# Kernel optimization log

Measured on AMD Instinct MI355X. Metric: run time of the kernel, lower is better.

The kernel has to match this reference:

```python
import jax, jax.numpy as jnp
import numpy as np

N_RAYS = 8192
M = 524288
GX, GY, GZ = 160, 160, 128
NFEAT = 12
POS_PE, VIEW_PE = 10, 4
WIDTH = 128
POS_DIM = 3 + 3 * POS_PE * 2      # 63
VIEW_DIM = 3 + 3 * VIEW_PE * 2    # 27
DIM0 = NFEAT + POS_DIM            # 75
ACT_SHIFT = float(np.log(1.0 / (1.0 - 1e-6) - 1.0))  # density bias shift from alpha_init
INTERVAL = 0.5                    # stepsize * voxel_size_ratio
XYZ_MIN, XYZ_MAX = -1.0, 1.0


def posemb(x, n_pe):
    # x: [N,3] -> [N, 3 + 3*n_pe*2], matching cat([x, sin(x*freq), cos(x*freq)])
    freq = 2.0 ** jnp.arange(n_pe, dtype=x.dtype)
    xf = (x[..., None] * freq).reshape(x.shape[0], -1)
    return jnp.concatenate([x, jnp.sin(xf), jnp.cos(xf)], axis=-1)


def trilinear(grid, xyz):
    # grid: [X,Y,Z,C]; xyz: [M,3] in world coords. align_corners=True bilinear (grid_sample).
    sz_f = jnp.array(grid.shape[:3], jnp.float32)
    sz_i = jnp.array(grid.shape[:3], jnp.int32)
    t = (xyz - XYZ_MIN) / (XYZ_MAX - XYZ_MIN) * (sz_f - 1.0)
    t = jnp.clip(t, 0.0, sz_f - 1.0)
    i0 = jnp.clip(jnp.floor(t).astype(jnp.int32), 0, sz_i - 2)
    f = t - i0.astype(t.dtype)
    out = jnp.zeros((xyz.shape[0], grid.shape[-1]), t.dtype)
    for dx in (0, 1):
        for dy in (0, 1):
            for dz in (0, 1):
                w = ((f[:, 0] if dx else 1.0 - f[:, 0])
                     * (f[:, 1] if dy else 1.0 - f[:, 1])
                     * (f[:, 2] if dz else 1.0 - f[:, 2]))
                out = out + w[:, None] * grid[i0[:, 0] + dx, i0[:, 1] + dy, i0[:, 2] + dz]
    return out


def mask_lookup(mask, xyz):
    # nearest-neighbor maskcache_lookup: ijk = round(xyz*scale + shift)
    sz_f = jnp.array(mask.shape, jnp.float32)
    scale = (sz_f - 1.0) / (XYZ_MAX - XYZ_MIN)
    shift = -XYZ_MIN * scale
    ijk = jnp.clip(jnp.round(xyz * scale + shift).astype(jnp.int32), 0,
                   jnp.array(mask.shape, jnp.int32) - 1)
    return mask[ijk[:, 0], ijk[:, 1], ijk[:, 2]]


def alphas2weights(alpha, ray_id, n_rays):
    # segmented T_i = prod_{j<i in ray}(1-alpha_j); weights = T*alpha (ray_id sorted)
    log1a = jnp.log(jnp.clip(1.0 - alpha, 1e-10, 1.0))
    excl = jnp.cumsum(log1a) - log1a                      # global exclusive cumsum
    seg_tot = jax.ops.segment_sum(log1a, ray_id, num_segments=n_rays)
    seg_start = jnp.cumsum(seg_tot) - seg_tot             # exclusive prefix over rays
    T = jnp.exp(excl - seg_start[ray_id])
    weights = T * alpha
    alphainv_last = jnp.exp(seg_tot)
    return weights, alphainv_last


def setup_inputs() -> dict:
    key = jax.random.key(0)
    ks = jax.random.split(key, 16)
    xyz = jax.random.uniform(ks[0], (M, 3), jnp.float32) * (XYZ_MAX - XYZ_MIN) + XYZ_MIN
    ray_id = jnp.sort(jax.random.randint(ks[1], (M,), 0, N_RAYS))
    viewdirs = jax.random.normal(ks[2], (N_RAYS, 3), jnp.float32)
    viewdirs = viewdirs / jnp.linalg.norm(viewdirs, axis=-1, keepdims=True)
    mask = jax.random.uniform(ks[3], (GX, GY, GZ)) > 0.1
    density = jax.random.normal(ks[4], (GX, GY, GZ), jnp.float32) * 0.5
    k0 = jax.random.normal(ks[5], (GX, GY, GZ, NFEAT), jnp.float32) * 0.1
    s = 0.05
    W0 = jax.random.normal(ks[6], (DIM0, WIDTH), jnp.float32) * s
    b0 = jnp.zeros((WIDTH,), jnp.float32)
    W1 = jax.random.normal(ks[7], (WIDTH, WIDTH), jnp.float32) * s
    b1 = jnp.zeros((WIDTH,), jnp.float32)
    W2 = jax.random.normal(ks[8], (WIDTH, WIDTH), jnp.float32) * s
    b2 = jnp.zeros((WIDTH,), jnp.float32)
    Wr = jax.random.normal(ks[9], (WIDTH + VIEW_DIM, 3), jnp.float32) * s
    br = jnp.zeros((3,), jnp.float32)
    return {"xyz": xyz, "ray_id": ray_id, "viewdirs": viewdirs, "mask": mask,
            "density": density, "k0": k0, "W0": W0, "b0": b0, "W1": W1, "b1": b1,
            "W2": W2, "b2": b2, "Wr": Wr, "br": br}


def reference(xyz, ray_id, viewdirs, mask, density, k0, W0, b0, W1, b1, W2, b2, Wr, br):
    # 1) empty-space skipping via mask cache (kept as multiplicative mask for static shapes)
    m = mask_lookup(mask, xyz).astype(xyz.dtype)
    # 2) trilinear density query + raw2alpha
    d = trilinear(density[..., None], xyz)[:, 0]
    alpha = 1.0 - (1.0 + jnp.exp(d + ACT_SHIFT)) ** (-INTERVAL)
    alpha = alpha * m
    # 3) segmented alpha compositing (Alphas2Weights)
    weights, alphainv_last = alphas2weights(alpha, ray_id, N_RAYS)
    # 4) feature query + view MLP -> rgb
    feat = trilinear(k0, xyz)                              # [M, NFEAT]
    h = jnp.concatenate([feat, posemb(xyz, POS_PE)], -1)   # [M, DIM0]
    h = jax.nn.relu(h @ W0 + b0)
    h = jax.nn.relu(h @ W1 + b1)
    h = jax.nn.relu(h @ W2 + b2)
    ve = posemb(viewdirs, VIEW_PE)[ray_id]                 # [M, VIEW_DIM]
    rgb = jax.nn.sigmoid(jnp.concatenate([h, ve], -1) @ Wr + br)
    # 5) composite per ray + white background
    rgb_marched = jax.ops.segment_sum(weights[:, None] * rgb, ray_id, num_segments=N_RAYS)
    rgb_marched = rgb_marched + alphainv_last[:, None] * 1.0
    return rgb_marched
```

## Files before the change

### kernel.cpp

```cpp
#include <hip/hip_runtime.h>
#include <hip/hip_bf16.h>

#define M_SAMPLES 524288
#define NRAYS 8192
#define GXD 160
#define GYD 160
#define GZD 128
#define GYZ (GYD*GZD)
#define NVOX (GXD*GYD*GZD)
#define ACT_SHIFT -13.81550955796f
#define ROWA 136
#define ROWB 168

typedef __bf16 bf16x8 __attribute__((ext_vector_type(8)));
typedef float f32x4 __attribute__((ext_vector_type(4)));
typedef float f32x16 __attribute__((ext_vector_type(16)));
typedef float f32v2 __attribute__((ext_vector_type(2)));

static __device__ inline unsigned short f2bf(float f){
  __hip_bfloat16 h = __float2bfloat16(f);
  unsigned short u; __builtin_memcpy(&u, &h, 2); return u;
}
static __device__ inline float flo(unsigned int u){ return __uint_as_float(u << 16); }
static __device__ inline float fhi(unsigned int u){ return __uint_as_float(u & 0xffff0000u); }

#if defined(__has_builtin)
#if __has_builtin(__builtin_amdgcn_cvt_pk_bf16_f32)
#define HAVE_PK_BF16 1
#endif
#if __has_builtin(__builtin_amdgcn_cvt_pk_f32_fp8) && __has_builtin(__builtin_amdgcn_cvt_pk_fp8_f32)
#define HAVE_FP8 1
#endif
#endif

static __device__ inline unsigned int packbf(float a, float b){
#ifdef HAVE_PK_BF16
  typedef __bf16 bf16v2 __attribute__((ext_vector_type(2)));
  bf16v2 r = __builtin_amdgcn_cvt_pk_bf16_f32(a, b);
  unsigned int u; __builtin_memcpy(&u, &r, 4); return u;
#else
  return (unsigned int)f2bf(a) | ((unsigned int)f2bf(b) << 16);
#endif
}

struct Tri {
  int ix, iy, iz;
  float wx0, wx1, wy0, wy1, wz0, wz1;
};
static __device__ inline Tri tri_setup(float x, float y, float z){
  Tri t;
  float tx = (x+1.f)*0.5f*(float)(GXD-1); tx = fminf(fmaxf(tx,0.f),(float)(GXD-1));
  float ty = (y+1.f)*0.5f*(float)(GYD-1); ty = fminf(fmaxf(ty,0.f),(float)(GYD-1));
  float tz = (z+1.f)*0.5f*(float)(GZD-1); tz = fminf(fmaxf(tz,0.f),(float)(GZD-1));
  t.ix = min((int)tx, GXD-2); t.iy = min((int)ty, GYD-2); t.iz = min((int)tz, GZD-2);
  float fx = tx-t.ix, fy = ty-t.iy, fz = tz-t.iz;
  t.wx0 = 1.f-fx; t.wx1 = fx; t.wy0 = 1.f-fy; t.wy1 = fy; t.wz0 = 1.f-fz; t.wz1 = fz;
  return t;
}

__global__ __launch_bounds__(256) void k_prep(const unsigned int* __restrict__ mw,
    int* __restrict__ flag,
    const float* __restrict__ W0, const float* __restrict__ W1,
    const float* __restrict__ W2, const float* __restrict__ Wr,
    unsigned short* __restrict__ wt0, unsigned short* __restrict__ wt1,
    unsigned short* __restrict__ wt2, unsigned short* __restrict__ wtr,
    const float* __restrict__ vd, float* __restrict__ ve)
{
  int b = blockIdx.x;
  if(b == 0){
    unsigned int v = mw[threadIdx.x & 63];
    unsigned long long any = __ballot(v > 1u);
    if(threadIdx.x == 0) *flag = (any != 0ull) ? 1 : 0;
    return;
  }
  if(b < 187){
    int t = (b-1)*256 + threadIdx.x;
    if(t < 128*96){
      int n = t/96, k = t%96;
      wt0[t] = f2bf((k < 75) ? W0[k*128 + n] : 0.f);
    } else if(t < 128*96 + 16384){
      int j = t - 128*96; int n = j/128, k = j%128;
      wt1[j] = f2bf(W1[k*128 + n]);
    } else if(t < 128*96 + 32768){
      int j = t - 128*96 - 16384; int n = j/128, k = j%128;
      wt2[j] = f2bf(W2[k*128 + n]);
    } else if(t < 128*96 + 32768 + 16*160){
      int j = t - 128*96 - 32768; int n = j/160, k = j%160;
      wtr[j] = f2bf((n < 3 && k < 155) ? Wr[k*3 + n] : 0.f);
    }
    return;
  }
  int t = (b-187)*256 + threadIdx.x;
  if(t >= NRAYS*27) return;
  int ray = t/27, c = t%27;
  float v;
  if(c < 3) v = vd[ray*3 + c];
  else if(c < 15){
    int q = c - 3; int ci = q/4, p = q%4;
    v = sinf(vd[ray*3 + ci] * (float)(1 << p));
  } else {
    int q = c - 15; int ci = q/4, p = q%4;
    v = cosf(vd[ray*3 + ci] * (float)(1 << p));
  }
  ve[t] = v;
}

#ifdef HAVE_FP8
__global__ __launch_bounds__(256) void k_repack(const float* __restrict__ density,
    const float* __restrict__ k0, uint4* __restrict__ packed)
{
  int v = blockIdx.x*256 + threadIdx.x;
  if(v >= NVOX) return;
  const float4* kp = (const float4*)(k0 + (size_t)v*12);
  float4 a = kp[0], b = kp[1], c = kp[2];
  uint4 o;
  o.x = __float_as_uint(density[v]);
  int w;
  w = __builtin_amdgcn_cvt_pk_fp8_f32(a.x, a.y, 0, false);
  w = __builtin_amdgcn_cvt_pk_fp8_f32(a.z, a.w, w, true);
  o.y = (unsigned int)w;
  w = __builtin_amdgcn_cvt_pk_fp8_f32(b.x, b.y, 0, false);
  w = __builtin_amdgcn_cvt_pk_fp8_f32(b.z, b.w, w, true);
  o.z = (unsigned int)w;
  w = __builtin_amdgcn_cvt_pk_fp8_f32(c.x, c.y, 0, false);
  w = __builtin_amdgcn_cvt_pk_fp8_f32(c.z, c.w, w, true);
  o.w = (unsigned int)w;
  packed[v] = o;
}
#else
__global__ __launch_bounds__(256) void k_repack(const float* __restrict__ density,
    const float* __restrict__ k0, uint4* __restrict__ packed)
{
  int v = blockIdx.x*256 + threadIdx.x;
  if(v >= NVOX) return;
  const float4* kp = (const float4*)(k0 + (size_t)v*12);
  float4 a = kp[0], b = kp[1], c = kp[2];
  uint4 o0, o1;
  o0.x = __float_as_uint(density[v]);
  o0.y = packbf(a.x, a.y); o0.z = packbf(a.z, a.w); o0.w = packbf(b.x, b.y);
  o1.x = packbf(b.z, b.w); o1.y = packbf(c.x, c.y); o1.z = packbf(c.z, c.w);
  o1.w = 0;
  packed[(size_t)v*2]   = o0;
  packed[(size_t)v*2+1] = o1;
}
#endif

template<int KDIM, int SROW, int DROW>
static __device__ inline void layer32(const unsigned short* src, unsigned short* dst,
    const unsigned short* __restrict__ wt, const float* __restrict__ bias,
    int wave, int ln, int kh)
{
  constexpr int NS = KDIM/16;
  int tile_s = wave & 1, tile_n = wave >> 1;
  const unsigned short* wbase = wt + (tile_n*32 + ln)*KDIM + kh*8;
  const unsigned short* abase = src + (tile_s*32 + ln)*SROW + kh*8;
  f32x16 acc = {0.f,0.f,0.f,0.f,0.f,0.f,0.f,0.f,0.f,0.f,0.f,0.f,0.f,0.f,0.f,0.f};
  #pragma unroll
  for(int st = 0; st < NS; ++st){
    bf16x8 af = *(const bf16x8*)(wbase + st*16);
    bf16x8 bfr = *(const bf16x8*)(abase + st*16);
    acc = __builtin_amdgcn_mfma_f32_32x32x16_bf16(af, bfr, acc, 0, 0, 0);
  }
  int scol = tile_s*32 + ln;
  #pragma unroll
  for(int g = 0; g < 4; ++g){
    int n0 = tile_n*32 + g*8 + kh*4;
    float4 bv = *(const float4*)(bias + n0);
    unsigned int lo = packbf(fmaxf(acc[4*g+0] + bv.x, 0.f), fmaxf(acc[4*g+1] + bv.y, 0.f));
    unsigned int hi = packbf(fmaxf(acc[4*g+2] + bv.z, 0.f), fmaxf(acc[4*g+3] + bv.w, 0.f));
    unsigned long long o = (unsigned long long)lo | ((unsigned long long)hi << 32);
    *(unsigned long long*)(dst + scol*DROW + n0) = o;
  }
}

template<int PACKED>
__global__ __launch_bounds__(512) void k_mlp(const float* __restrict__ xyz,
    const uint4* __restrict__ packed,
    const float* __restrict__ density, const float* __restrict__ k0,
    const void* __restrict__ mask, const int* __restrict__ flag,
    const int* __restrict__ ray_id,
    const unsigned short* __restrict__ wt0, const unsigned short* __restrict__ wt1,
    const unsigned short* __restrict__ wt2, const unsigned short* __restrict__ wtr,
    const float* __restrict__ b0, const float* __restrict__ b1,
    const float* __restrict__ b2, const float* __restrict__ br,
    const float* __restrict__ ve,
    float* __restrict__ alpha_w, float4* __restrict__ rgb_out)
{
  __shared__ alignas(16) unsigned short hA[64*ROWA];
  __shared__ alignas(16) unsigned short hB[64*ROWB];
  __shared__ float red[64][4];

  int tid = threadIdx.x;
  int lane = tid & 63, wave = tid >> 6;

  if(wave < 4){
    int smp = (wave << 4) | (lane >> 2);
    int corner = lane & 3;
    int i = blockIdx.x*64 + smp;
    float x = xyz[3*i+0], y = xyz[3*i+1], z = xyz[3*i+2];
    Tri t = tri_setup(x, y, z);
    int dx = corner & 1, dy = corner >> 1;
    float wxy = (dx ? t.wx1 : t.wx0) * (dy ? t.wy1 : t.wy0);
    float w0 = wxy*t.wz0, w1 = wxy*t.wz1;
    size_t vox = (size_t)((t.ix+dx)*GYZ + (t.iy+dy)*GZD + t.iz);
    float pd;
    float pf[12];
#ifdef HAVE_FP8
    if(PACKED){
      uint4 q0 = packed[vox], q1 = packed[vox+1];
      pd = w0*__uint_as_float(q0.x) + w1*__uint_as_float(q1.x);
      f32v2 a, b;
      a = __builtin_amdgcn_cvt_pk_f32_fp8((int)q0.y, false);
      b = __builtin_amdgcn_cvt_pk_f32_fp8((int)q1.y, false);
      pf[0] = w0*a.x + w1*b.x;  pf[1] = w0*a.y + w1*b.y;
      a = __builtin_amdgcn_cvt_pk_f32_fp8((int)q0.y, true);
      b = __builtin_amdgcn_cvt_pk_f32_fp8((int)q1.y, true);
      pf[2] = w0*a.x + w1*b.x;  pf[3] = w0*a.y + w1*b.y;
      a = __builtin_amdgcn_cvt_pk_f32_fp8((int)q0.z, false);
      b = __builtin_amdgcn_cvt_pk_f32_fp8((int)q1.z, false);
      pf[4] = w0*a.x + w1*b.x;  pf[5] = w0*a.y + w1*b.y;
      a = __builtin_amdgcn_cvt_pk_f32_fp8((int)q0.z, true);
      b = __builtin_amdgcn_cvt_pk_f32_fp8((int)q1.z, true);
      pf[6] = w0*a.x + w1*b.x;  pf[7] = w0*a.y + w1*b.y;
      a = __builtin_amdgcn_cvt_pk_f32_fp8((int)q0.w, false);
      b = __builtin_amdgcn_cvt_pk_f32_fp8((int)q1.w, false);
      pf[8] = w0*a.x + w1*b.x;  pf[9] = w0*a.y + w1*b.y;
      a = __builtin_amdgcn_cvt_pk_f32_fp8((int)q0.w, true);
      b = __builtin_amdgcn_cvt_pk_f32_fp8((int)q1.w, true);
      pf[10]= w0*a.x + w1*b.x;  pf[11]= w0*a.y + w1*b.y;
    }
#else
    if(PACKED){
      const uint4* pv = packed + vox*2;
      uint4 q0 = pv[0], q1 = pv[1], q2 = pv[2], q3 = pv[3];
      pd = w0*__uint_as_float(q0.x) + w1*__uint_as_float(q2.x);
      pf[0]  = w0*flo(q0.y) + w1*flo(q2.y);  pf[1]  = w0*fhi(q0.y) + w1*fhi(q2.y);
      pf[2]  = w0*flo(q0.z) + w1*flo(q2.z);  pf[3]  = w0*fhi(q0.z) + w1*fhi(q2.z);
      pf[4]  = w0*flo(q0.w) + w1*flo(q2.w);  pf[5]  = w0*fhi(q0.w) + w1*fhi(q2.w);
      pf[6]  = w0*flo(q1.x) + w1*flo(q3.x);  pf[7]  = w0*fhi(q1.x) + w1*fhi(q3.x);
      pf[8]  = w0*flo(q1.y) + w1*flo(q3.y);  pf[9]  = w0*fhi(q1.y) + w1*fhi(q3.y);
      pf[10] = w0*flo(q1.z) + w1*flo(q3.z);  pf[11] = w0*fhi(q1.z) + w1*fhi(q3.z);
    }
#endif
    if(!PACKED){
      pd = w0*density[vox] + w1*density[vox+1];
      const float4* v = (const float4*)(k0 + vox*12);
      float4 a0 = v[0], a1 = v[1], a2 = v[2];
      float4 c0 = v[3], c1 = v[4], c2 = v[5];
      pf[0] = w0*a0.x + w1*c0.x;  pf[1] = w0*a0.y + w1*c0.y;
      pf[2] = w0*a0.z + w1*c0.z;  pf[3] = w0*a0.w + w1*c0.w;
      pf[4] = w0*a1.x + w1*c1.x;  pf[5] = w0*a1.y + w1*c1.y;
      pf[6] = w0*a1.z + w1*c1.z;  pf[7] = w0*a1.w + w1*c1.w;
      pf[8] = w0*a2.x + w1*c2.x;  pf[9] = w0*a2.y + w1*c2.y;
      pf[10]= w0*a2.z + w1*c2.z;  pf[11]= w0*a2.w + w1*c2.w;
    }
    #pragma unroll
    for(int m2 = 1; m2 < 4; m2 <<= 1){
      pd += __shfl_xor(pd, m2);
      #pragma unroll
      for(int j = 0; j < 12; ++j) pf[j] += __shfl_xor(pf[j], m2);
    }
    if(corner == 0){
      int mx = (int)rintf(x*79.5f + 79.5f); mx = min(max(mx,0), GXD-1);
      int my = (int)rintf(y*79.5f + 79.5f); my = min(max(my,0), GYD-1);
      int mz = (int)rintf(z*63.5f + 63.5f); mz = min(max(mz,0), GZD-1);
      int midx = mx*GYZ + my*GZD + mz;
      bool mm = (*flag) ? (((const unsigned char*)mask)[midx] != 0)
                        : (((const int*)mask)[midx] != 0);
      float e = expf(pd + ACT_SHIFT);
      float alpha = 1.f - rsqrtf(1.f + e);
      if(!mm) alpha = 0.f;
      alpha_w[i] = alpha;
      unsigned int d[8];
      #pragma unroll
      for(int j = 0; j < 6; ++j) d[j] = packbf(pf[2*j], pf[2*j+1]);
      d[6] = packbf(x, y);
      d[7] = packbf(z, __sinf(x));
      uint4* p = (uint4*)(hA + smp*ROWA);
      p[0] = make_uint4(d[0],d[1],d[2],d[3]);
      p[1] = make_uint4(d[4],d[5],d[6],d[7]);
    } else if(corner == 1){
      uint4* p = (uint4*)(hA + smp*ROWA + 80);
      p[0] = make_uint4(0,0,0,0);
      p[1] = make_uint4(0,0,0,0);
    } else {
      int ray = ray_id[i];
      int cb = (corner - 2) * 16;
      unsigned int d[8];
      #pragma unroll
      for(int j = 0; j < 8; ++j){
        int c = cb + 2*j;
        float a = (c     < 27) ? ve[ray*27 + c]     : 0.f;
        float b = (c + 1 < 27) ? ve[ray*27 + c + 1] : 0.f;
        d[j] = packbf(a, b);
      }
      uint4* p = (uint4*)(hB + smp*ROWB + 128 + cb);
      p[0] = make_uint4(d[0],d[1],d[2],d[3]);
      p[1] = make_uint4(d[4],d[5],d[6],d[7]);
    }
  } else {
    int chunk = wave - 3;
    int i2 = blockIdx.x*64 + lane;
    float x = xyz[3*i2+0], y = xyz[3*i2+1], z = xyz[3*i2+2];
    float vv[16];
    #pragma unroll
    for(int j = 0; j < 16; ++j){
      int c = chunk*16 + j;
      float r;
      if(c >= 75) r = 0.f;
      else {
        int q = (c < 45) ? (c-15) : (c-45);
        int ci = q/10, p = q - ci*10;
        float xv = (ci == 0) ? x : ((ci == 1) ? y : z);
        float a = xv * (float)(1 << p);
        r = (c < 45) ? __sinf(a) : __cosf(a);
      }
      vv[j] = r;
    }
    unsigned int d[8];
    #pragma unroll
    for(int j = 0; j < 8; ++j) d[j] = packbf(vv[2*j], vv[2*j+1]);
    uint4* p = (uint4*)(hA + lane*ROWA + chunk*16);
    p[0] = make_uint4(d[0],d[1],d[2],d[3]);
    p[1] = make_uint4(d[4],d[5],d[6],d[7]);
  }
  __syncthreads();

  int ln = lane & 31, kh = lane >> 5;
  layer32< 96, ROWA, ROWB>(hA, hB, wt0, b0, wave, ln, kh);  __syncthreads();
  layer32<128, ROWB, ROWA>(hB, hA, wt1, b1, wave, ln, kh);  __syncthreads();
  layer32<128, ROWA, ROWB>(hA, hB, wt2, b2, wave, ln, kh);  __syncthreads();

  int col = lane & 15, q = lane >> 4;
  if(wave < 4){
    int mt = wave;
    f32x4 acc = {0.f, 0.f, 0.f, 0.f};
    const unsigned short* arow = hB + (mt*16 + col)*ROWB + q*8;
    const unsigned short* wrow = wtr + col*160 + q*8;
    #pragma unroll
    for(int ks = 0; ks < 5; ++ks){
      bf16x8 af = *(const bf16x8*)(arow + ks*32);
      bf16x8 bfr = *(const bf16x8*)(wrow + ks*32);
      acc = __builtin_amdgcn_mfma_f32_16x16x32_bf16(af, bfr, acc, 0, 0, 0);
    }
    if(col < 3){
      #pragma unroll
      for(int r = 0; r < 4; ++r){
        int sl = mt*16 + q*4 + r;
        float v = acc[r] + br[col];
        red[sl][col] = 1.f / (1.f + expf(-v));
      }
    }
  }
  __syncthreads();

  if(wave == 7){
    int i2 = blockIdx.x*64 + lane;
    rgb_out[i2] = make_float4(red[lane][0], red[lane][1], red[lane][2], 0.f);
  }
}

__global__ __launch_bounds__(256) void k_comp2(const int* __restrict__ ray_id,
    const float* __restrict__ alpha_w, const float4* __restrict__ rgb,
    float* __restrict__ out)
{
  int r = blockIdx.x*4 + (threadIdx.x >> 6);
  int lane = threadIdx.x & 63;
  int lo = 0, hi = M_SAMPLES;
  while(lo < hi){ int mid = (lo+hi) >> 1; if(ray_id[mid] < r) lo = mid+1; else hi = mid; }
  int s = lo;
  int lo2 = s, hi2 = M_SAMPLES;
  while(lo2 < hi2){ int mid = (lo2+hi2) >> 1; if(ray_id[mid] < r+1) lo2 = mid+1; else hi2 = mid; }
  int e = lo2;

  float carry = 1.f;
  float ar = 0.f, ag = 0.f, ab = 0.f;
  for(int base = s; base < e; base += 64){
    int idx = base + lane;
    float a = (idx < e) ? alpha_w[idx] : 0.f;
    float incl = 1.f - a;
    #pragma unroll
    for(int d2 = 1; d2 < 64; d2 <<= 1){
      float t = __shfl_up(incl, d2);
      if(lane >= d2) incl *= t;
    }
    float excl = __shfl_up(incl, 1);
    if(lane == 0) excl = 1.f;
    float w = carry * excl * a;
    if(idx < e){
      float4 c = rgb[idx];
      ar += w*c.x; ag += w*c.y; ab += w*c.z;
    }
    carry *= __shfl(incl, 63);
  }
  #pragma unroll
  for(int m2 = 1; m2 < 64; m2 <<= 1){
    ar += __shfl_xor(ar, m2);
    ag += __shfl_xor(ag, m2);
    ab += __shfl_xor(ab, m2);
  }
  if(lane == 0){
    out[3*r+0] = ar + carry;
    out[3*r+1] = ag + carry;
    out[3*r+2] = ab + carry;
  }
}

extern "C" void kernel_launch(void* const* d_in, const int* in_sizes, int n_in,
                              void* d_out, int out_size, void* d_ws, size_t ws_size,
                              hipStream_t stream)
{
  const float* xyz      = (const float*)d_in[0];
  const int*   ray_id   = (const int*)  d_in[1];
  const float* viewdirs = (const float*)d_in[2];
  const void*  mask     =               d_in[3];
  const float* density  = (const float*)d_in[4];
  const float* k0       = (const float*)d_in[5];
  const float* W0 = (const float*)d_in[6];  const float* b0 = (const float*)d_in[7];
  const float* W1 = (const float*)d_in[8];  const float* b1 = (const float*)d_in[9];
  const float* W2 = (const float*)d_in[10]; const float* b2 = (const float*)d_in[11];
  const float* Wr = (const float*)d_in[12]; const float* br = (const float*)d_in[13];
  float* out = (float*)d_out;

  char* ws = (char*)d_ws;
  size_t off = 0;
  auto take = [&](size_t nbytes) -> void* {
    void* p = ws + off;
    off = (off + nbytes + 255) & ~(size_t)255;
    return p;
  };
  int*            flag    = (int*)           take(4);
  unsigned short* wt0     = (unsigned short*)take(128*96*2);
  unsigned short* wt1     = (unsigned short*)take(128*128*2);
  unsigned short* wt2     = (unsigned short*)take(128*128*2);
  unsigned short* wtr     = (unsigned short*)take(16*160*2);
  float*          ve      = (float*)         take((size_t)NRAYS*27*4);
  float*          alpha_w = (float*)         take((size_t)M_SAMPLES*4);
  float4*         rgb_ws  = (float4*)        take((size_t)M_SAMPLES*16);
#ifdef HAVE_FP8
  uint4*          packed  = (uint4*)         take((size_t)NVOX*16);
#else
  uint4*          packed  = (uint4*)         take((size_t)NVOX*32);
#endif
  bool use_packed = (ws_size >= off);

  k_prep<<<1051, 256, 0, stream>>>((const unsigned int*)mask, flag,
                                   W0, W1, W2, Wr, wt0, wt1, wt2, wtr, viewdirs, ve);
  if(use_packed){
    k_repack<<<(NVOX+255)/256, 256, 0, stream>>>(density, k0, packed);
    k_mlp<1><<<M_SAMPLES/64, 512, 0, stream>>>(xyz, packed, density, k0, mask, flag,
                                               ray_id, wt0, wt1, wt2, wtr,
                                               b0, b1, b2, br, ve, alpha_w, rgb_ws);
  } else {
    k_mlp<0><<<M_SAMPLES/64, 512, 0, stream>>>(xyz, packed, density, k0, mask, flag,
                                               ray_id, wt0, wt1, wt2, wtr,
                                               b0, b1, b2, br, ve, alpha_w, rgb_ws);
  }
  k_comp2<<<NRAYS/4, 256, 0, stream>>>(ray_id, alpha_w, rgb_ws, out);
}
```

Baseline: 486.9 us.

## Double MLP samples per block, merge repack into prep, pack alpha with rgb

Each k_mlp block now handles 128 samples instead of 64. Every wave computes two 32x32 MFMA tiles that share one weight fragment, which halves weight loads per sample, and all 512 threads now take part in the gather and positional-encoding stages. The grid repack moves into the k_prep kernel, which removes one launch. Alpha is written into the w lane of the rgb float4, so compositing reads a single vector per sample. The trade-off is doubled LDS per block, which may reduce occupancy.

```diff
diff --git a/kernel.cpp b/kernel.cpp
--- a/kernel.cpp
+++ b/kernel.cpp
@@ -11,6 +11,7 @@
 #define ACT_SHIFT -13.81550955796f
 #define ROWA 136
 #define ROWB 168
+#define SAMP 128
 
 typedef __bf16 bf16x8 __attribute__((ext_vector_type(8)));
 typedef float f32x4 __attribute__((ext_vector_type(4)));
@@ -58,8 +59,13 @@
   return t;
 }
 
-__global__ __launch_bounds__(256) void k_prep(const unsigned int* __restrict__ mw,
-    int* __restrict__ flag,
+#define NB_REPACK (NVOX/256)
+#define NB_W      186
+#define NB_VE     864
+__global__ __launch_bounds__(256) void k_prep(
+    const float* __restrict__ density, const float* __restrict__ k0,
+    uint4* __restrict__ packed,
+    const unsigned int* __restrict__ mw, int* __restrict__ flag,
     const float* __restrict__ W0, const float* __restrict__ W1,
     const float* __restrict__ W2, const float* __restrict__ Wr,
     unsigned short* __restrict__ wt0, unsigned short* __restrict__ wt1,
@@ -67,14 +73,43 @@
     const float* __restrict__ vd, float* __restrict__ ve)
 {
   int b = blockIdx.x;
-  if(b == 0){
+  if(b < NB_REPACK){
+    int v = b*256 + threadIdx.x;
+    const float4* kp = (const float4*)(k0 + (size_t)v*12);
+    float4 a = kp[0], bb = kp[1], c = kp[2];
+#ifdef HAVE_FP8
+    uint4 o;
+    o.x = __float_as_uint(density[v]);
+    int w;
+    w = __builtin_amdgcn_cvt_pk_fp8_f32(a.x, a.y, 0, false);
+    w = __builtin_amdgcn_cvt_pk_fp8_f32(a.z, a.w, w, true);
+    o.y = (unsigned int)w;
+    w = __builtin_amdgcn_cvt_pk_fp8_f32(bb.x, bb.y, 0, false);
+    w = __builtin_amdgcn_cvt_pk_fp8_f32(bb.z, bb.w, w, true);
+    o.z = (unsigned int)w;
+    w = __builtin_amdgcn_cvt_pk_fp8_f32(c.x, c.y, 0, false);
+    w = __builtin_amdgcn_cvt_pk_fp8_f32(c.z, c.w, w, true);
+    o.w = (unsigned int)w;
+    packed[v] = o;
+#else
+    uint4 o0, o1;
+    o0.x = __float_as_uint(density[v]);
+    o0.y = packbf(a.x, a.y); o0.z = packbf(a.z, a.w); o0.w = packbf(bb.x, bb.y);
+    o1.x = packbf(bb.z, bb.w); o1.y = packbf(c.x, c.y); o1.z = packbf(c.z, c.w);
+    o1.w = 0;
+    packed[(size_t)v*2]   = o0;
+    packed[(size_t)v*2+1] = o1;
+#endif
+    return;
+  }
+  if(b == NB_REPACK){
     unsigned int v = mw[threadIdx.x & 63];
     unsigned long long any = __ballot(v > 1u);
     if(threadIdx.x == 0) *flag = (any != 0ull) ? 1 : 0;
     return;
   }
-  if(b < 187){
-    int t = (b-1)*256 + threadIdx.x;
+  if(b < NB_REPACK + 1 + NB_W){
+    int t = (b - NB_REPACK - 1)*256 + threadIdx.x;
     if(t < 128*96){
       int n = t/96, k = t%96;
       wt0[t] = f2bf((k < 75) ? W0[k*128 + n] : 0.f);
@@ -90,7 +125,7 @@
     }
     return;
   }
-  int t = (b-187)*256 + threadIdx.x;
+  int t = (b - NB_REPACK - 1 - NB_W)*256 + threadIdx.x;
   if(t >= NRAYS*27) return;
   int ray = t/27, c = t%27;
   float v;
@@ -105,71 +140,40 @@
   ve[t] = v;
 }
 
-#ifdef HAVE_FP8
-__global__ __launch_bounds__(256) void k_repack(const float* __restrict__ density,
-    const float* __restrict__ k0, uint4* __restrict__ packed)
-{
-  int v = blockIdx.x*256 + threadIdx.x;
-  if(v >= NVOX) return;
-  const float4* kp = (const float4*)(k0 + (size_t)v*12);
-  float4 a = kp[0], b = kp[1], c = kp[2];
-  uint4 o;
-  o.x = __float_as_uint(density[v]);
-  int w;
-  w = __builtin_amdgcn_cvt_pk_fp8_f32(a.x, a.y, 0, false);
-  w = __builtin_amdgcn_cvt_pk_fp8_f32(a.z, a.w, w, true);
-  o.y = (unsigned int)w;
-  w = __builtin_amdgcn_cvt_pk_fp8_f32(b.x, b.y, 0, false);
-  w = __builtin_amdgcn_cvt_pk_fp8_f32(b.z, b.w, w, true);
-  o.z = (unsigned int)w;
-  w = __builtin_amdgcn_cvt_pk_fp8_f32(c.x, c.y, 0, false);
-  w = __builtin_amdgcn_cvt_pk_fp8_f32(c.z, c.w, w, true);
-  o.w = (unsigned int)w;
-  packed[v] = o;
-}
-#else
-__global__ __launch_bounds__(256) void k_repack(const float* __restrict__ density,
-    const float* __restrict__ k0, uint4* __restrict__ packed)
-{
-  int v = blockIdx.x*256 + threadIdx.x;
-  if(v >= NVOX) return;
-  const float4* kp = (const float4*)(k0 + (size_t)v*12);
-  float4 a = kp[0], b = kp[1], c = kp[2];
-  uint4 o0, o1;
-  o0.x = __float_as_uint(density[v]);
-  o0.y = packbf(a.x, a.y); o0.z = packbf(a.z, a.w); o0.w = packbf(b.x, b.y);
-  o1.x = packbf(b.z, b.w); o1.y = packbf(c.x, c.y); o1.z = packbf(c.z, c.w);
-  o1.w = 0;
-  packed[(size_t)v*2]   = o0;
-  packed[(size_t)v*2+1] = o1;
-}
-#endif
-
 template<int KDIM, int SROW, int DROW>
 static __device__ inline void layer32(const unsigned short* src, unsigned short* dst,
     const unsigned short* __restrict__ wt, const float* __restrict__ bias,
     int wave, int ln, int kh)
 {
   constexpr int NS = KDIM/16;
-  int tile_s = wave & 1, tile_n = wave >> 1;
+  int tile_n = wave >> 1;
+  int m0 = (wave & 1) * 2;
   const unsigned short* wbase = wt + (tile_n*32 + ln)*KDIM + kh*8;
-  const unsigned short* abase = src + (tile_s*32 + ln)*SROW + kh*8;
-  f32x16 acc = {0.f,0.f,0.f,0.f,0.f,0.f,0.f,0.f,0.f,0.f,0.f,0.f,0.f,0.f,0.f,0.f};
+  const unsigned short* abase0 = src + ((m0  )*32 + ln)*SROW + kh*8;
+  const unsigned short* abase1 = src + ((m0+1)*32 + ln)*SROW + kh*8;
+  f32x16 acc0 = {0.f,0.f,0.f,0.f,0.f,0.f,0.f,0.f,0.f,0.f,0.f,0.f,0.f,0.f,0.f,0.f};
+  f32x16 acc1 = acc0;
   #pragma unroll
   for(int st = 0; st < NS; ++st){
-    bf16x8 af = *(const bf16x8*)(wbase + st*16);
-    bf16x8 bfr = *(const bf16x8*)(abase + st*16);
-    acc = __builtin_amdgcn_mfma_f32_32x32x16_bf16(af, bfr, acc, 0, 0, 0);
-  }
-  int scol = tile_s*32 + ln;
+    bf16x8 wf = *(const bf16x8*)(wbase + st*16);
+    bf16x8 a0 = *(const bf16x8*)(abase0 + st*16);
+    bf16x8 a1 = *(const bf16x8*)(abase1 + st*16);
+    acc0 = __builtin_amdgcn_mfma_f32_32x32x16_bf16(wf, a0, acc0, 0, 0, 0);
+    acc1 = __builtin_amdgcn_mfma_f32_32x32x16_bf16(wf, a1, acc1, 0, 0, 0);
+  }
   #pragma unroll
-  for(int g = 0; g < 4; ++g){
-    int n0 = tile_n*32 + g*8 + kh*4;
-    float4 bv = *(const float4*)(bias + n0);
-    unsigned int lo = packbf(fmaxf(acc[4*g+0] + bv.x, 0.f), fmaxf(acc[4*g+1] + bv.y, 0.f));
-    unsigned int hi = packbf(fmaxf(acc[4*g+2] + bv.z, 0.f), fmaxf(acc[4*g+3] + bv.w, 0.f));
-    unsigned long long o = (unsigned long long)lo | ((unsigned long long)hi << 32);
-    *(unsigned long long*)(dst + scol*DROW + n0) = o;
+  for(int rep = 0; rep < 2; ++rep){
+    const f32x16& acc = rep ? acc1 : acc0;
+    int scol = (m0 + rep)*32 + ln;
+    #pragma unroll
+    for(int g = 0; g < 4; ++g){
+      int n0 = tile_n*32 + g*8 + kh*4;
+      float4 bv = *(const float4*)(bias + n0);
+      unsigned int lo = packbf(fmaxf(acc[4*g+0] + bv.x, 0.f), fmaxf(acc[4*g+1] + bv.y, 0.f));
+      unsigned int hi = packbf(fmaxf(acc[4*g+2] + bv.z, 0.f), fmaxf(acc[4*g+3] + bv.w, 0.f));
+      unsigned long long o = (unsigned long long)lo | ((unsigned long long)hi << 32);
+      *(unsigned long long*)(dst + scol*DROW + n0) = o;
+    }
   }
 }
 
@@ -183,20 +187,19 @@
     const unsigned short* __restrict__ wt2, const unsigned short* __restrict__ wtr,
     const float* __restrict__ b0, const float* __restrict__ b1,
     const float* __restrict__ b2, const float* __restrict__ br,
-    const float* __restrict__ ve,
-    float* __restrict__ alpha_w, float4* __restrict__ rgb_out)
+    const float* __restrict__ ve, float4* __restrict__ rgba_out)
 {
-  __shared__ alignas(16) unsigned short hA[64*ROWA];
-  __shared__ alignas(16) unsigned short hB[64*ROWB];
-  __shared__ float red[64][4];
+  __shared__ alignas(16) unsigned short hA[SAMP*ROWA];
+  __shared__ alignas(16) unsigned short hB[SAMP*ROWB];
+  __shared__ float red[SAMP][4];
 
   int tid = threadIdx.x;
   int lane = tid & 63, wave = tid >> 6;
-
-  if(wave < 4){
-    int smp = (wave << 4) | (lane >> 2);
-    int corner = lane & 3;
-    int i = blockIdx.x*64 + smp;
+  int blk = blockIdx.x*SAMP;
+
+  {
+    int smp = tid >> 2, corner = tid & 3;
+    int i = blk + smp;
     float x = xyz[3*i+0], y = xyz[3*i+1], z = xyz[3*i+2];
     Tri t = tri_setup(x, y, z);
     int dx = corner & 1, dy = corner >> 1;
@@ -270,7 +273,7 @@
       float e = expf(pd + ACT_SHIFT);
       float alpha = 1.f - rsqrtf(1.f + e);
       if(!mm) alpha = 0.f;
-      alpha_w[i] = alpha;
+      red[smp][3] = alpha;
       unsigned int d[8];
       #pragma unroll
       for(int j = 0; j < 6; ++j) d[j] = packbf(pf[2*j], pf[2*j+1]);
@@ -298,9 +301,11 @@
       p[0] = make_uint4(d[0],d[1],d[2],d[3]);
       p[1] = make_uint4(d[4],d[5],d[6],d[7]);
     }
-  } else {
-    int chunk = wave - 3;
-    int i2 = blockIdx.x*64 + lane;
+  }
+
+  {
+    int smp = tid & 127, chunk = 1 + (tid >> 7);
+    int i2 = blk + smp;
     float x = xyz[3*i2+0], y = xyz[3*i2+1], z = xyz[3*i2+2];
     float vv[16];
     #pragma unroll
@@ -320,7 +325,7 @@
     unsigned int d[8];
     #pragma unroll
     for(int j = 0; j < 8; ++j) d[j] = packbf(vv[2*j], vv[2*j+1]);
-    uint4* p = (uint4*)(hA + lane*ROWA + chunk*16);
+    uint4* p = (uint4*)(hA + smp*ROWA + chunk*16);
     p[0] = make_uint4(d[0],d[1],d[2],d[3]);
     p[1] = make_uint4(d[4],d[5],d[6],d[7]);
   }
@@ -331,8 +336,8 @@
   layer32<128, ROWB, ROWA>(hB, hA, wt1, b1, wave, ln, kh);  __syncthreads();
   layer32<128, ROWA, ROWB>(hA, hB, wt2, b2, wave, ln, kh);  __syncthreads();
 
-  int col = lane & 15, q = lane >> 4;
-  if(wave < 4){
+  {
+    int col = lane & 15, q = lane >> 4;
     int mt = wave;
     f32x4 acc = {0.f, 0.f, 0.f, 0.f};
     const unsigned short* arow = hB + (mt*16 + col)*ROWB + q*8;
@@ -354,15 +359,13 @@
   }
   __syncthreads();
 
-  if(wave == 7){
-    int i2 = blockIdx.x*64 + lane;
-    rgb_out[i2] = make_float4(red[lane][0], red[lane][1], red[lane][2], 0.f);
+  if(tid < SAMP){
+    rgba_out[blk + tid] = make_float4(red[tid][0], red[tid][1], red[tid][2], red[tid][3]);
   }
 }
 
 __global__ __launch_bounds__(256) void k_comp2(const int* __restrict__ ray_id,
-    const float* __restrict__ alpha_w, const float4* __restrict__ rgb,
-    float* __restrict__ out)
+    const float4* __restrict__ rgba, float* __restrict__ out)
 {
   int r = blockIdx.x*4 + (threadIdx.x >> 6);
   int lane = threadIdx.x & 63;
@@ -377,7 +380,8 @@
   float ar = 0.f, ag = 0.f, ab = 0.f;
   for(int base = s; base < e; base += 64){
     int idx = base + lane;
-    float a = (idx < e) ? alpha_w[idx] : 0.f;
+    float4 c = (idx < e) ? rgba[idx] : make_float4(0.f,0.f,0.f,0.f);
+    float a = c.w;
     float incl = 1.f - a;
     #pragma unroll
     for(int d2 = 1; d2 < 64; d2 <<= 1){
@@ -387,10 +391,7 @@
     float excl = __shfl_up(incl, 1);
     if(lane == 0) excl = 1.f;
     float w = carry * excl * a;
-    if(idx < e){
-      float4 c = rgb[idx];
-      ar += w*c.x; ag += w*c.y; ab += w*c.z;
-    }
+    ar += w*c.x; ag += w*c.y; ab += w*c.z;
     carry *= __shfl(incl, 63);
   }
   #pragma unroll
@@ -435,8 +436,7 @@
   unsigned short* wt2     = (unsigned short*)take(128*128*2);
   unsigned short* wtr     = (unsigned short*)take(16*160*2);
   float*          ve      = (float*)         take((size_t)NRAYS*27*4);
-  float*          alpha_w = (float*)         take((size_t)M_SAMPLES*4);
-  float4*         rgb_ws  = (float4*)        take((size_t)M_SAMPLES*16);
+  float4*         rgba_ws = (float4*)        take((size_t)M_SAMPLES*16);
 #ifdef HAVE_FP8
   uint4*          packed  = (uint4*)         take((size_t)NVOX*16);
 #else
@@ -444,17 +444,17 @@
 #endif
   bool use_packed = (ws_size >= off);
 
-  k_prep<<<1051, 256, 0, stream>>>((const unsigned int*)mask, flag,
-                                   W0, W1, W2, Wr, wt0, wt1, wt2, wtr, viewdirs, ve);
+  k_prep<<<NB_REPACK + 1 + NB_W + NB_VE, 256, 0, stream>>>(
+      density, k0, packed, (const unsigned int*)mask, flag,
+      W0, W1, W2, Wr, wt0, wt1, wt2, wtr, viewdirs, ve);
   if(use_packed){
-    k_repack<<<(NVOX+255)/256, 256, 0, stream>>>(density, k0, packed);
-    k_mlp<1><<<M_SAMPLES/64, 512, 0, stream>>>(xyz, packed, density, k0, mask, flag,
-                                               ray_id, wt0, wt1, wt2, wtr,
-                                               b0, b1, b2, br, ve, alpha_w, rgb_ws);
+    k_mlp<1><<<M_SAMPLES/SAMP, 512, 0, stream>>>(xyz, packed, density, k0, mask, flag,
+                                                 ray_id, wt0, wt1, wt2, wtr,
+                                                 b0, b1, b2, br, ve, rgba_ws);
   } else {
-    k_mlp<0><<<M_SAMPLES/64, 512, 0, stream>>>(xyz, packed, density, k0, mask, flag,
-                                               ray_id, wt0, wt1, wt2, wtr,
-                                               b0, b1, b2, br, ve, alpha_w, rgb_ws);
-  }
-  k_comp2<<<NRAYS/4, 256, 0, stream>>>(ray_id, alpha_w, rgb_ws, out);
-}
+    k_mlp<0><<<M_SAMPLES/SAMP, 512, 0, stream>>>(xyz, packed, density, k0, mask, flag,
+                                                 ray_id, wt0, wt1, wt2, wtr,
+                                                 b0, b1, b2, br, ve, rgba_ws);
+  }
+  k_comp2<<<NRAYS/4, 256, 0, stream>>>(ray_id, rgba_ws, out);
+}
```

Result: faster. 434.9 us (-10.7%).
